# Kernel tuning notes

Measured on AMD Instinct MI355X. Metric: run time of the kernel, lower is better.

The kernel has to match this reference:

```python
import jax, jax.numpy as jnp
import numpy as np

WINDOW_SIZE = 7
L = 255.0
C1 = (0.01 * L) ** 2
C2 = (0.03 * L) ** 2


def _box_filter(x, window):
    # x: [B,1,H,W], window: [1,1,k,k] (uniform 1/k^2). VALID conv, groups=1.
    return jax.lax.conv_general_dilated(
        x, window, window_strides=(1, 1), padding='VALID',
        dimension_numbers=('NCHW', 'OIHW', 'NCHW'))


def setup_inputs() -> dict:
    key = jax.random.key(0)
    k1, k2 = jax.random.split(key)
    shape = (16, 1, 1080, 1920)
    img1 = jax.random.uniform(k1, shape, dtype=jnp.float32) * L
    img2 = jax.random.uniform(k2, shape, dtype=jnp.float32) * L
    window = jnp.ones((1, 1, WINDOW_SIZE, WINDOW_SIZE), dtype=jnp.float32) / (WINDOW_SIZE * WINDOW_SIZE)
    return {"img1": img1, "img2": img2, "window": window}


def reference(img1, img2, window):
    mu1 = _box_filter(img1, window)
    mu2 = _box_filter(img2, window)
    mu1_sq = mu1 * mu1
    mu2_sq = mu2 * mu2
    mu1_mu2 = mu1 * mu2
    sigma1_sq = _box_filter(img1 * img1, window) - mu1_sq
    sigma2_sq = _box_filter(img2 * img2, window) - mu2_sq
    sigma12 = _box_filter(img1 * img2, window) - mu1_mu2
    v1 = 2.0 * sigma12 + C2
    v2 = sigma1_sq + sigma2_sq + C2
    ssim_map = (2.0 * mu1_mu2 + C1) * v1 / ((mu1_sq + mu2_sq + C1) * v2)
    return jnp.mean(ssim_map)
```

## Files before the change

kernel.cpp:

```cpp
#include <hip/hip_runtime.h>


constexpr int W_IN = 1920, H_IN = 1080;
constexpr int WOUT = W_IN - 6;
constexpr int HOUT = H_IN - 6;
constexpr int NBATCH = 16;
constexpr int WCOLS = 122;
constexpr int TW = 4 * WCOLS;
constexpr int TH = 71;
constexpr int NBX = 4, NBY = 16;
constexpr int NBLK = NBX * NBY * NBATCH;

constexpr float C1f = 6.5025f;
constexpr float C2f = 58.5225f;
constexpr float INV49 = 1.0f / 49.0f;

__device__ __forceinline__ float bperm(int addr, float v) {
  return __int_as_float(__builtin_amdgcn_ds_bpermute(addr, __float_as_int(v)));
}

__global__ __attribute__((amdgpu_flat_work_group_size(256, 256),
                          amdgpu_waves_per_eu(4, 4)))
void ssim_kernel(const float* __restrict__ img1, const float* __restrict__ img2,
                 double* __restrict__ partial) {
  __shared__ float2 ring[2 * 7 * 256];
  __shared__ float wsum[4];

  const int t = threadIdx.x;
  float2* const rA = ring + t;
  float2* const rB = ring + 7 * 256 + t;

  const int lane = t & 63;
  const int xw = blockIdx.x * TW + (t >> 6) * WCOLS;
  const int y0 = blockIdx.y * TH;
  const size_t ib = (size_t)blockIdx.z * (size_t)(H_IN * W_IN);
  const float* __restrict__ p1 = img1 + ib;
  const float* __restrict__ p2 = img2 + ib;

  const int gcol = min(xw + 2 * lane, W_IN - 2);
  const int up1 = ((lane + 1) & 63) << 2;
  const int up2 = ((lane + 2) & 63) << 2;
  const int up3 = ((lane + 3) & 63) << 2;
  const bool lv = lane < 61;
  const bool m0 = lv && (xw + 2 * lane + 0 < WOUT);
  const bool m1 = lv && (xw + 2 * lane + 1 < WOUT);

  const float2 z2 = make_float2(0.f, 0.f);
#pragma unroll
  for (int j = 0; j < 7; ++j) { rA[j * 256] = z2; rB[j * 256] = z2; }

  float V1_0 = 0.f, V1_1 = 0.f;
  float V2_0 = 0.f, V2_1 = 0.f;
  float V3_0 = 0.f, V3_1 = 0.f;
  float V4_0 = 0.f, V4_1 = 0.f;
  float V5_0 = 0.f, V5_1 = 0.f;

  float accv = 0.f;

  float2 Aa = *(const float2*)(p1 + (size_t)y0 * W_IN + gcol);
  float2 Ab = *(const float2*)(p2 + (size_t)y0 * W_IN + gcol);
  float2 Ba, Bb;
  int gyn = y0 + 1;
  int oy = y0;

#define EPI1(VA, VB, VAA, VBB, VAB, MASK)                                   \
  {                                                                         \
    const float mu1 = (VA) * INV49, mu2 = (VB) * INV49;                     \
    const float mu1s = mu1 * mu1, mu2s = mu2 * mu2, mu12 = mu1 * mu2;       \
    const float sg1 = fmaf((VAA), INV49, -mu1s);                            \
    const float sg2 = fmaf((VBB), INV49, -mu2s);                            \
    const float sg12 = fmaf((VAB), INV49, -mu12);                           \
    const float v1 = fmaf(2.f, sg12, C2f);                                  \
    const float v2 = sg1 + sg2 + C2f;                                       \
    const float num = fmaf(2.f, mu12, C1f) * v1;                            \
    const float den = (mu1s + mu2s + C1f) * v2;                             \
    const float ss = num * __builtin_amdgcn_rcpf(den);                      \
    accv += (MASK) ? ss : 0.f;                                              \
  }

#define HQ(Q)                                                               \
    const float s1_##Q = bperm(up1, H##Q);                                  \
    const float s2_##Q = bperm(up2, H##Q);                                  \
    const float s3_##Q = bperm(up3, H##Q);                                  \
    const float f3_##Q = bperm(up3, V##Q##_0);                              \
    const float sh_##Q = s1_##Q + s2_##Q;                                   \
    const float h0_##Q = (H##Q + sh_##Q) + f3_##Q;                          \
    const float h1_##Q = (V##Q##_1 + sh_##Q) + s3_##Q;

#define STEP(J, CAa, CAb, NAa, NAb, DO_EPI)                                 \
  {                                                                         \
    NAa = *(const float2*)(p1 + (size_t)gyn * W_IN + gcol);                 \
    NAb = *(const float2*)(p2 + (size_t)gyn * W_IN + gcol);                 \
    gyn = min(gyn + 1, H_IN - 1);                                           \
    const float2 oa = rA[(J) * 256];                                        \
    const float2 ob = rB[(J) * 256];                                        \
    rA[(J) * 256] = CAa;                                                    \
    rB[(J) * 256] = CAb;                                                    \
    V1_0 = (V1_0 + CAa.x) - oa.x;  V1_1 = (V1_1 + CAa.y) - oa.y;            \
    V2_0 = (V2_0 + CAb.x) - ob.x;  V2_1 = (V2_1 + CAb.y) - ob.y;            \
    V3_0 = fmaf(CAa.x, CAa.x, V3_0); V3_0 = fmaf(-oa.x, oa.x, V3_0);        \
    V3_1 = fmaf(CAa.y, CAa.y, V3_1); V3_1 = fmaf(-oa.y, oa.y, V3_1);        \
    V4_0 = fmaf(CAb.x, CAb.x, V4_0); V4_0 = fmaf(-ob.x, ob.x, V4_0);        \
    V4_1 = fmaf(CAb.y, CAb.y, V4_1); V4_1 = fmaf(-ob.y, ob.y, V4_1);        \
    V5_0 = fmaf(CAa.x, CAb.x, V5_0); V5_0 = fmaf(-oa.x, ob.x, V5_0);        \
    V5_1 = fmaf(CAa.y, CAb.y, V5_1); V5_1 = fmaf(-oa.y, ob.y, V5_1);        \
    if (DO_EPI) {                                                           \
      if (oy < HOUT) {                                                      \
        const float H1 = V1_0 + V1_1;                                       \
        const float H2 = V2_0 + V2_1;                                       \
        const float H3 = V3_0 + V3_1;                                       \
        const float H4 = V4_0 + V4_1;                                       \
        const float H5 = V5_0 + V5_1;                                       \
        HQ(1) HQ(2) HQ(3) HQ(4) HQ(5)                                       \
        EPI1(h0_1, h0_2, h0_3, h0_4, h0_5, m0)                              \
        EPI1(h1_1, h1_2, h1_3, h1_4, h1_5, m1)                              \
      }                                                                     \
      ++oy;                                                                 \
    }                                                                       \
  }

  STEP(0, Aa, Ab, Ba, Bb, false)
  STEP(1, Ba, Bb, Aa, Ab, false)
  STEP(2, Aa, Ab, Ba, Bb, false)
  STEP(3, Ba, Bb, Aa, Ab, false)
  STEP(4, Aa, Ab, Ba, Bb, false)
  STEP(5, Ba, Bb, Aa, Ab, false)
  STEP(6, Aa, Ab, Ba, Bb, true)
  for (int gp = 0; gp < 5; ++gp) {
    STEP(0, Ba, Bb, Aa, Ab, true)
    STEP(1, Aa, Ab, Ba, Bb, true)
    STEP(2, Ba, Bb, Aa, Ab, true)
    STEP(3, Aa, Ab, Ba, Bb, true)
    STEP(4, Ba, Bb, Aa, Ab, true)
    STEP(5, Aa, Ab, Ba, Bb, true)
    STEP(6, Ba, Bb, Aa, Ab, true)
    STEP(0, Aa, Ab, Ba, Bb, true)
    STEP(1, Ba, Bb, Aa, Ab, true)
    STEP(2, Aa, Ab, Ba, Bb, true)
    STEP(3, Ba, Bb, Aa, Ab, true)
    STEP(4, Aa, Ab, Ba, Bb, true)
    STEP(5, Ba, Bb, Aa, Ab, true)
    STEP(6, Aa, Ab, Ba, Bb, true)
  }
#undef STEP
#undef HQ
#undef EPI1

#pragma unroll
  for (int off = 32; off > 0; off >>= 1) accv += __shfl_down(accv, off);
  if ((t & 63) == 0) wsum[t >> 6] = accv;
  __syncthreads();
  if (t == 0) {
    const int bid = blockIdx.x + NBX * (blockIdx.y + NBY * blockIdx.z);
    partial[bid] = (double)wsum[0] + (double)wsum[1] +
                   (double)wsum[2] + (double)wsum[3];
  }
}

__global__ __launch_bounds__(256)
void finalize_kernel(const double* __restrict__ partial,
                     float* __restrict__ out) {
  const int tid = threadIdx.x;
  double s = 0.0;
  for (int i = tid; i < NBLK; i += 256) s += partial[i];
#pragma unroll
  for (int off = 32; off > 0; off >>= 1) s += __shfl_down(s, off);
  __shared__ double ws[4];
  if ((tid & 63) == 0) ws[tid >> 6] = s;
  __syncthreads();
  if (tid == 0) {
    const double tot = ws[0] + ws[1] + ws[2] + ws[3];
    out[0] = (float)(tot / ((double)NBATCH * (double)HOUT * (double)WOUT));
  }
}

extern "C" void kernel_launch(void* const* d_in, const int* in_sizes, int n_in,
                              void* d_out, int out_size, void* d_ws, size_t ws_size,
                              hipStream_t stream) {
  const float* img1 = (const float*)d_in[0];
  const float* img2 = (const float*)d_in[1];
  double* partial = (double*)d_ws;
  dim3 grid(NBX, NBY, NBATCH);
  hipLaunchKernelGGL(ssim_kernel, grid, dim3(256), 0, stream, img1, img2,
                     partial);
  hipLaunchKernelGGL(finalize_kernel, dim3(1), dim3(256), 0, stream, partial,
                     (float*)d_out);
}
```

Baseline: 289.3 us.

## Replace LDS row ring with global reloads of outgoing rows, halve tile height

Removes the shared-memory ring buffer that held the last seven input rows. Each outgoing row is now re-read from global memory (expected to hit cache) and subtracted from the running vertical sums. Tile height drops from 71 to 35 rows with more blocks, and the waves-per-EU hint rises from 4 to 8 for higher occupancy. The cost is twice the global load traffic per step and a larger share of redundant 6-row halo work per tile.

```diff
diff --git a/kernel.cpp b/kernel.cpp
--- a/kernel.cpp
+++ b/kernel.cpp
@@ -7,8 +7,8 @@
 constexpr int NBATCH = 16;
 constexpr int WCOLS = 122;
 constexpr int TW = 4 * WCOLS;
-constexpr int TH = 71;
-constexpr int NBX = 4, NBY = 16;
+constexpr int TH = 35;
+constexpr int NBX = 4, NBY = 31;
 constexpr int NBLK = NBX * NBY * NBATCH;
 
 constexpr float C1f = 6.5025f;
@@ -20,16 +20,12 @@
 }
 
 __global__ __attribute__((amdgpu_flat_work_group_size(256, 256),
-                          amdgpu_waves_per_eu(4, 4)))
+                          amdgpu_waves_per_eu(8, 8)))
 void ssim_kernel(const float* __restrict__ img1, const float* __restrict__ img2,
                  double* __restrict__ partial) {
-  __shared__ float2 ring[2 * 7 * 256];
   __shared__ float wsum[4];
 
   const int t = threadIdx.x;
-  float2* const rA = ring + t;
-  float2* const rB = ring + 7 * 256 + t;
-
   const int lane = t & 63;
   const int xw = blockIdx.x * TW + (t >> 6) * WCOLS;
   const int y0 = blockIdx.y * TH;
@@ -45,22 +41,18 @@
   const bool m0 = lv && (xw + 2 * lane + 0 < WOUT);
   const bool m1 = lv && (xw + 2 * lane + 1 < WOUT);
 
-  const float2 z2 = make_float2(0.f, 0.f);
-#pragma unroll
-  for (int j = 0; j < 7; ++j) { rA[j * 256] = z2; rB[j * 256] = z2; }
-
   float V1_0 = 0.f, V1_1 = 0.f;
   float V2_0 = 0.f, V2_1 = 0.f;
   float V3_0 = 0.f, V3_1 = 0.f;
   float V4_0 = 0.f, V4_1 = 0.f;
   float V5_0 = 0.f, V5_1 = 0.f;
-
   float accv = 0.f;
 
   float2 Aa = *(const float2*)(p1 + (size_t)y0 * W_IN + gcol);
   float2 Ab = *(const float2*)(p2 + (size_t)y0 * W_IN + gcol);
-  float2 Ba, Bb;
+  float2 Ba, Bb, Pa, Pb, Qa, Qb;
   int gyn = y0 + 1;
+  int gyo = y0 + 1;
   int oy = y0;
 
 #define EPI1(VA, VB, VAA, VBB, VAB, MASK)                                   \
@@ -87,62 +79,76 @@
     const float h0_##Q = (H##Q + sh_##Q) + f3_##Q;                          \
     const float h1_##Q = (V##Q##_1 + sh_##Q) + s3_##Q;
 
-#define STEP(J, CAa, CAb, NAa, NAb, DO_EPI)                                 \
+#define VUPD_ADD(CAa, CAb)                                                  \
+    V1_0 += CAa.x;                   V1_1 += CAa.y;                         \
+    V2_0 += CAb.x;                   V2_1 += CAb.y;                         \
+    V3_0 = fmaf(CAa.x, CAa.x, V3_0); V3_1 = fmaf(CAa.y, CAa.y, V3_1);       \
+    V4_0 = fmaf(CAb.x, CAb.x, V4_0); V4_1 = fmaf(CAb.y, CAb.y, V4_1);       \
+    V5_0 = fmaf(CAa.x, CAb.x, V5_0); V5_1 = fmaf(CAa.y, CAb.y, V5_1);
+
+#define VUPD_SUB(COa, COb)                                                  \
+    V1_0 -= COa.x;                     V1_1 -= COa.y;                       \
+    V2_0 -= COb.x;                     V2_1 -= COb.y;                       \
+    V3_0 = fmaf(-COa.x, COa.x, V3_0);  V3_1 = fmaf(-COa.y, COa.y, V3_1);    \
+    V4_0 = fmaf(-COb.x, COb.x, V4_0);  V4_1 = fmaf(-COb.y, COb.y, V4_1);    \
+    V5_0 = fmaf(-COa.x, COb.x, V5_0);  V5_1 = fmaf(-COa.y, COb.y, V5_1);
+
+#define DO_EPI_BLOCK                                                        \
+    if (oy < HOUT) {                                                        \
+      const float H1 = V1_0 + V1_1;                                         \
+      const float H2 = V2_0 + V2_1;                                         \
+      const float H3 = V3_0 + V3_1;                                         \
+      const float H4 = V4_0 + V4_1;                                         \
+      const float H5 = V5_0 + V5_1;                                         \
+      HQ(1) HQ(2) HQ(3) HQ(4) HQ(5)                                         \
+      EPI1(h0_1, h0_2, h0_3, h0_4, h0_5, m0)                                \
+      EPI1(h1_1, h1_2, h1_3, h1_4, h1_5, m1)                                \
+    }                                                                       \
+    ++oy;
+
+#define STEPW(CAa, CAb, NAa, NAb, DO_EPI)                                   \
   {                                                                         \
     NAa = *(const float2*)(p1 + (size_t)gyn * W_IN + gcol);                 \
     NAb = *(const float2*)(p2 + (size_t)gyn * W_IN + gcol);                 \
     gyn = min(gyn + 1, H_IN - 1);                                           \
-    const float2 oa = rA[(J) * 256];                                        \
-    const float2 ob = rB[(J) * 256];                                        \
-    rA[(J) * 256] = CAa;                                                    \
-    rB[(J) * 256] = CAb;                                                    \
-    V1_0 = (V1_0 + CAa.x) - oa.x;  V1_1 = (V1_1 + CAa.y) - oa.y;            \
-    V2_0 = (V2_0 + CAb.x) - ob.x;  V2_1 = (V2_1 + CAb.y) - ob.y;            \
-    V3_0 = fmaf(CAa.x, CAa.x, V3_0); V3_0 = fmaf(-oa.x, oa.x, V3_0);        \
-    V3_1 = fmaf(CAa.y, CAa.y, V3_1); V3_1 = fmaf(-oa.y, oa.y, V3_1);        \
-    V4_0 = fmaf(CAb.x, CAb.x, V4_0); V4_0 = fmaf(-ob.x, ob.x, V4_0);        \
-    V4_1 = fmaf(CAb.y, CAb.y, V4_1); V4_1 = fmaf(-ob.y, ob.y, V4_1);        \
-    V5_0 = fmaf(CAa.x, CAb.x, V5_0); V5_0 = fmaf(-oa.x, ob.x, V5_0);        \
-    V5_1 = fmaf(CAa.y, CAb.y, V5_1); V5_1 = fmaf(-oa.y, ob.y, V5_1);        \
-    if (DO_EPI) {                                                           \
-      if (oy < HOUT) {                                                      \
-        const float H1 = V1_0 + V1_1;                                       \
-        const float H2 = V2_0 + V2_1;                                       \
-        const float H3 = V3_0 + V3_1;                                       \
-        const float H4 = V4_0 + V4_1;                                       \
-        const float H5 = V5_0 + V5_1;                                       \
-        HQ(1) HQ(2) HQ(3) HQ(4) HQ(5)                                       \
-        EPI1(h0_1, h0_2, h0_3, h0_4, h0_5, m0)                              \
-        EPI1(h1_1, h1_2, h1_3, h1_4, h1_5, m1)                              \
-      }                                                                     \
-      ++oy;                                                                 \
-    }                                                                       \
+    VUPD_ADD(CAa, CAb)                                                      \
+    if (DO_EPI) { DO_EPI_BLOCK }                                            \
   }
 
-  STEP(0, Aa, Ab, Ba, Bb, false)
-  STEP(1, Ba, Bb, Aa, Ab, false)
-  STEP(2, Aa, Ab, Ba, Bb, false)
-  STEP(3, Ba, Bb, Aa, Ab, false)
-  STEP(4, Aa, Ab, Ba, Bb, false)
-  STEP(5, Ba, Bb, Aa, Ab, false)
-  STEP(6, Aa, Ab, Ba, Bb, true)
-  for (int gp = 0; gp < 5; ++gp) {
-    STEP(0, Ba, Bb, Aa, Ab, true)
-    STEP(1, Aa, Ab, Ba, Bb, true)
-    STEP(2, Ba, Bb, Aa, Ab, true)
-    STEP(3, Aa, Ab, Ba, Bb, true)
-    STEP(4, Ba, Bb, Aa, Ab, true)
-    STEP(5, Aa, Ab, Ba, Bb, true)
-    STEP(6, Ba, Bb, Aa, Ab, true)
-    STEP(0, Aa, Ab, Ba, Bb, true)
-    STEP(1, Ba, Bb, Aa, Ab, true)
-    STEP(2, Aa, Ab, Ba, Bb, true)
-    STEP(3, Ba, Bb, Aa, Ab, true)
-    STEP(4, Aa, Ab, Ba, Bb, true)
-    STEP(5, Ba, Bb, Aa, Ab, true)
-    STEP(6, Aa, Ab, Ba, Bb, true)
+#define STEPM(CAa, CAb, NAa, NAb, COa, COb, NOa, NOb)                       \
+  {                                                                         \
+    NAa = *(const float2*)(p1 + (size_t)gyn * W_IN + gcol);                 \
+    NAb = *(const float2*)(p2 + (size_t)gyn * W_IN + gcol);                 \
+    gyn = min(gyn + 1, H_IN - 1);                                           \
+    {                                                                       \
+      const int yo = min(gyo, H_IN - 1);                                    \
+      NOa = *(const float2*)(p1 + (size_t)yo * W_IN + gcol);                \
+      NOb = *(const float2*)(p2 + (size_t)yo * W_IN + gcol);                \
+      ++gyo;                                                                \
+    }                                                                       \
+    VUPD_ADD(CAa, CAb)                                                      \
+    VUPD_SUB(COa, COb)                                                      \
+    DO_EPI_BLOCK                                                            \
   }
-#undef STEP
+
+  STEPW(Aa, Ab, Ba, Bb, false)
+  STEPW(Ba, Bb, Aa, Ab, false)
+  STEPW(Aa, Ab, Ba, Bb, false)
+  STEPW(Ba, Bb, Aa, Ab, false)
+  STEPW(Aa, Ab, Ba, Bb, false)
+  STEPW(Ba, Bb, Aa, Ab, false)
+  STEPW(Aa, Ab, Ba, Bb, true)
+  Pa = *(const float2*)(p1 + (size_t)y0 * W_IN + gcol);
+  Pb = *(const float2*)(p2 + (size_t)y0 * W_IN + gcol);
+  for (int gp = 0; gp < 17; ++gp) {
+    STEPM(Ba, Bb, Aa, Ab, Pa, Pb, Qa, Qb)
+    STEPM(Aa, Ab, Ba, Bb, Qa, Qb, Pa, Pb)
+  }
+#undef STEPM
+#undef STEPW
+#undef DO_EPI_BLOCK
+#undef VUPD_SUB
+#undef VUPD_ADD
 #undef HQ
 #undef EPI1
 
```

After: 294.6 us. No clear change (+1.8%).
